# Performance work log

Measured on AMD Instinct MI355X. Metric: run time of the kernel, lower is better.

Reference implementation:

```python
import jax, jax.numpy as jnp
import numpy as np

D_MODEL = 4096
D_HIDDEN = 32768
BATCH = 2048
K = 128
N_DEAD = 2048


def _ln(x, eps=1e-5):
    # torch .std() is unbiased (ddof=1)
    mu = jnp.mean(x, axis=-1, keepdims=True)
    xc = x - mu
    std = jnp.std(x, axis=-1, keepdims=True, ddof=1)
    return xc / (std + eps), mu, std


def _topk_activation(x, k):
    # topk over last dim, relu values, scatter back into zeros
    vals, idx = jax.lax.top_k(x, k)          # [B, k]
    vals = jax.nn.relu(vals)
    rows = jnp.arange(x.shape[0])[:, None]    # [B, 1]
    return jnp.zeros_like(x).at[rows, idx].set(vals)


def setup_inputs() -> dict:
    key = jax.random.key(0)
    k1, k2 = jax.random.split(key)
    x = jax.random.normal(k1, (BATCH, D_MODEL), dtype=jnp.float32)
    # kaiming-uniform-ish encoder init
    bound = 1.0 / np.sqrt(D_MODEL)
    w_enc = jax.random.uniform(k2, (D_MODEL, D_HIDDEN), dtype=jnp.float32,
                               minval=-bound, maxval=bound)
    w_dec = w_enc.T
    w_dec = w_dec / jnp.linalg.norm(w_dec, axis=0, keepdims=True)
    b_enc = jnp.zeros((D_HIDDEN,), dtype=jnp.float32)
    b_pre = jnp.zeros((D_MODEL,), dtype=jnp.float32)
    # fixed dead-neuron mask with exactly N_DEAD dead latents
    dm = np.zeros((D_HIDDEN,), dtype=bool)
    rng = np.random.default_rng(0)
    dm[rng.choice(D_HIDDEN, size=N_DEAD, replace=False)] = True
    dead_mask = jnp.asarray(dm)
    return {"x": x, "w_enc": w_enc, "w_dec": w_dec, "b_enc": b_enc,
            "b_pre": b_pre, "dead_mask": dead_mask, "num_dead": N_DEAD}


def reference(x, w_enc, w_dec, b_enc, b_pre, dead_mask, num_dead):
    xn, mu, std = _ln(x)
    xc = xn - b_pre
    pre_acts = xc @ w_enc + b_enc                 # [B, d_hidden]
    latents = _topk_activation(pre_acts, K)
    recons = latents @ w_dec + b_pre              # [B, d_model]
    recons = recons * std + mu
    # auxk dead-neuron path (num_dead is a static python int)
    k_aux = min(x.shape[-1] // 2, num_dead)
    auxk_latents = jnp.where(dead_mask[None, :], pre_acts, -jnp.inf)
    auxk_acts = _topk_activation(auxk_latents, k_aux)
    auxk = auxk_acts @ w_dec + b_pre
    auxk = auxk * std + mu
    return recons, auxk, num_dead
```

## Files before the change

### kernel.cpp

```cpp
#include <hip/hip_runtime.h>
#include <math.h>

#define D_MODEL  4096
#define D_HIDDEN 32768
#define BATCH    2048
#define KSEL     128
#define NDEAD    2048
#define TIECAP   256

typedef short s16x8 __attribute__((ext_vector_type(8)));
typedef float f32x4 __attribute__((ext_vector_type(4)));

__device__ __forceinline__ unsigned int fkey(float f) {
    unsigned int u = __float_as_uint(f);
    return (u & 0x80000000u) ? ~u : (u | 0x80000000u);
}
__device__ __forceinline__ unsigned short f2bf(float f) {
    unsigned int u = __float_as_uint(f);
    u += 0x7FFFu + ((u >> 16) & 1u);
    return (unsigned short)(u >> 16);
}
__device__ __forceinline__ float bf2f(unsigned short h) {
    return __uint_as_float(((unsigned int)h) << 16);
}
__device__ __forceinline__ unsigned int key16x2(unsigned int u) {
    const unsigned int s = (u >> 15) & 0x10001u;
    const unsigned int mask = s * 0xFFFFu;
    return (u ^ mask) | (~mask & 0x80008000u);
}
__device__ __forceinline__ float unkey16(unsigned int k) {
    const unsigned int u = (k & 0x8000u) ? (k & 0x7FFFu) : (~k & 0xFFFFu);
    return __uint_as_float(u << 16);
}
__device__ __forceinline__ void async_copy16(void* lds_dst, const void* gsrc) {
    __builtin_amdgcn_global_load_lds(
        (const __attribute__((address_space(1))) unsigned int*)gsrc,
        (__attribute__((address_space(3))) unsigned int*)lds_dst,
        16, 0, 0);
}

__global__ __launch_bounds__(256) void ln_kernel(const float* __restrict__ x,
        double* __restrict__ mu, double* __restrict__ stdv, double* __restrict__ sinv)
{
    const int row = blockIdx.x;
    const int tid = threadIdx.x;
    const float* xr = x + (size_t)row * D_MODEL;
    float xv[16];
#pragma unroll
    for (int i = 0; i < 16; ++i) xv[i] = xr[tid + 256 * i];
    double s = 0.0;
#pragma unroll
    for (int i = 0; i < 16; ++i) s += (double)xv[i];
    __shared__ double red[4];
    __shared__ double sh_mu;
    const int lane = tid & 63, wid = tid >> 6;
#pragma unroll
    for (int off = 32; off > 0; off >>= 1) s += __shfl_down(s, off, 64);
    if (lane == 0) red[wid] = s;
    __syncthreads();
    if (tid == 0) sh_mu = (red[0] + red[1] + red[2] + red[3]) / (double)D_MODEL;
    __syncthreads();
    const double m = sh_mu;
    double s2 = 0.0;
#pragma unroll
    for (int i = 0; i < 16; ++i) { double d = (double)xv[i] - m; s2 += d * d; }
#pragma unroll
    for (int off = 32; off > 0; off >>= 1) s2 += __shfl_down(s2, off, 64);
    __syncthreads();
    if (lane == 0) red[wid] = s2;
    __syncthreads();
    if (tid == 0) {
        double var = (red[0] + red[1] + red[2] + red[3]) / (double)(D_MODEL - 1);
        double sd = sqrt(var);
        mu[row] = m;
        stdv[row] = sd;
        sinv[row] = 1.0 / (sd + 1e-5);
    }
}

__global__ void dead_scan_kernel(const unsigned char* __restrict__ mask8,
                                 int* __restrict__ dead_idx, int* __restrict__ dead_cnt,
                                 const int* __restrict__ num_dead_in, float* __restrict__ out_last)
{
    const int lane = threadIdx.x;
    int c = 0;
    for (int j = lane; j < D_HIDDEN; j += 64) c += (mask8[j] != 0);
#pragma unroll
    for (int off = 32; off > 0; off >>= 1) c += __shfl_down(c, off, 64);
    const int total_u8 = __shfl(c, 0, 64);
    const bool u8mode = (total_u8 == NDEAD);
    const int* mask32 = (const int*)mask8;
    int cnt = 0;
    for (int base = 0; base < D_HIDDEN; base += 64) {
        const int j = base + lane;
        const bool d = u8mode ? (mask8[j] != 0) : (mask32[j] != 0);
        const unsigned long long b = __ballot(d);
        const int pre = __popcll(b & ((1ull << lane) - 1ull));
        if (d && (cnt + pre) < NDEAD) dead_idx[cnt + pre] = j;
        cnt += __popcll(b);
    }
    const int cc = cnt > NDEAD ? NDEAD : cnt;
    if (lane == 0) {
        *dead_cnt = cc;
        *out_last = (float)(*num_dead_in);
    }
    for (int t = cc + lane; t < NDEAD; t += 64) dead_idx[t] = 0;
}

__global__ __launch_bounds__(256) void asplit_kernel(
    const float* __restrict__ x, const double* __restrict__ mu, const double* __restrict__ sinv,
    const float* __restrict__ b_pre, unsigned short* __restrict__ Ahp)
{
    const int row = blockIdx.x, tid = threadIdx.x;
    const double m = mu[row], si = sinv[row];
    const float* xr = x + (size_t)row * D_MODEL;
#pragma unroll
    for (int i = 0; i < 4; ++i) {
        const int j = (i * 256 + tid) * 4;
        const float4 xv = *(const float4*)(xr + j);
        const float4 bp = *(const float4*)(b_pre + j);
        float v[4];
        v[0] = (float)(((double)xv.x - m) * si) - bp.x;
        v[1] = (float)(((double)xv.y - m) * si) - bp.y;
        v[2] = (float)(((double)xv.z - m) * si) - bp.z;
        v[3] = (float)(((double)xv.w - m) * si) - bp.w;
        uint2 hw;
        hw.x = (unsigned)f2bf(v[0]) | ((unsigned)f2bf(v[1]) << 16);
        hw.y = (unsigned)f2bf(v[2]) | ((unsigned)f2bf(v[3]) << 16);
        *(uint2*)(Ahp + (size_t)row * D_MODEL + j) = hw;
    }
}

__global__ __launch_bounds__(256) void bsplit_kernel(
    const float* __restrict__ w_enc, unsigned short* __restrict__ Bhp)
{
    __shared__ float t[32][33];
    const int bk = blockIdx.x * 32;
    const int bn = blockIdx.y * 32;
    const int tid = threadIdx.x;
    const int lr = tid >> 3, lc4 = (tid & 7) * 4;
    const float4 v = *(const float4*)(w_enc + (size_t)(bk + lr) * D_HIDDEN + bn + lc4);
    t[lr][lc4 + 0] = v.x; t[lr][lc4 + 1] = v.y; t[lr][lc4 + 2] = v.z; t[lr][lc4 + 3] = v.w;
    __syncthreads();
    float o[4];
#pragma unroll
    for (int j = 0; j < 4; ++j) o[j] = t[lc4 + j][lr];
    uint2 hw;
    hw.x = (unsigned)f2bf(o[0]) | ((unsigned)f2bf(o[1]) << 16);
    hw.y = (unsigned)f2bf(o[2]) | ((unsigned)f2bf(o[3]) << 16);
    *(uint2*)(Bhp + (size_t)(bn + lr) * D_MODEL + bk + lc4) = hw;
}

__global__ __launch_bounds__(256) void wencT_kernel(
    const float* __restrict__ w_enc, float* __restrict__ wT)
{
    __shared__ float t[32][33];
    const int bk = blockIdx.x * 32;
    const int bn = blockIdx.y * 32;
    const int tid = threadIdx.x;
    const int lr = tid >> 3, lc4 = (tid & 7) * 4;
    const float4 v = *(const float4*)(w_enc + (size_t)(bk + lr) * D_HIDDEN + bn + lc4);
    t[lr][lc4 + 0] = v.x; t[lr][lc4 + 1] = v.y; t[lr][lc4 + 2] = v.z; t[lr][lc4 + 3] = v.w;
    __syncthreads();
    const int j = tid >> 3, i4 = (tid & 7) * 4;
    float4 o;
    o.x = t[i4 + 0][j]; o.y = t[i4 + 1][j]; o.z = t[i4 + 2][j]; o.w = t[i4 + 3][j];
    *(float4*)(wT + (size_t)(bn + j) * D_MODEL + bk + i4) = o;
}

template<int EPI>
__global__ __launch_bounds__(512) void mm256_kernel(
    const unsigned short* __restrict__ A, const unsigned short* __restrict__ B,
    const int kdim, const int ntiles_x,
    const float* __restrict__ bias_n,
    const double* __restrict__ muv, const double* __restrict__ stdvv,
    void* __restrict__ outp, const long ostride)
{
    __shared__ unsigned short lds[2 * 4 * 8192];
    const int tid = threadIdx.x;
    const int lane = tid & 63, wid = tid >> 6;
    const int cpx = gridDim.x >> 3;
    const int orig = blockIdx.x;
    const int wg = (orig & 7) * cpx + (orig >> 3);
    const int m0 = (wg % ntiles_x) * 256;
    const int n0 = (wg / ntiles_x) * 256;
    const int wm = (wid >> 2) * 128;
    const int wn = (wid & 3) * 64;
    const int fr = lane & 15, kq = lane >> 4;
    const int swr = (fr >> 1) & 3;
    const int qg = (lane & 3) ^ ((lane >> 3) & 3);
    const int qo = (kq ^ swr) * 8;

    f32x4 acc[8][4];
#pragma unroll
    for (int i = 0; i < 8; ++i)
#pragma unroll
        for (int j = 0; j < 4; ++j) acc[i][j] = (f32x4){0.f, 0.f, 0.f, 0.f};

    const unsigned short* sH0[4];
    int dH0[4];
#pragma unroll
    for (int j = 0; j < 4; ++j) {
        const int g = wid * 4 + j;
        const int is_b = g >> 4;
        const int sr = g & 15;
        const unsigned short* gp = is_b ? B : A;
        const int t0 = is_b ? n0 : m0;
        sH0[j] = gp + (size_t)(t0 + sr * 16 + (lane >> 2)) * kdim + qg * 8;
        dH0[j] = (is_b ? 2 : 0) * 8192 + sr * 512;
    }

    const int NT = kdim >> 6;
#pragma unroll
    for (int j = 0; j < 4; ++j) async_copy16(lds + dH0[j], sH0[j]);
#pragma unroll
    for (int j = 0; j < 4; ++j) async_copy16(lds + 8192 + dH0[j], sH0[j] + 32);
    if (NT > 1) {
#pragma unroll
        for (int j = 0; j < 4; ++j) async_copy16(lds + 32768 + dH0[j], sH0[j] + 64);
    }

    for (int t = 0; t < NT; ++t) {
        const int cur = t & 1;
        unsigned short* bb = (unsigned short*)lds + cur * 32768;
        unsigned short* nb = (unsigned short*)lds + (cur ^ 1) * 32768;
        const int k1 = (t + 1) << 6;
        const int k2 = (t + 2) << 6;

        if (t < NT - 1) { asm volatile("s_waitcnt vmcnt(8)" ::: "memory"); }
        else            { asm volatile("s_waitcnt vmcnt(4)" ::: "memory"); }
        asm volatile("s_barrier" ::: "memory");
        __builtin_amdgcn_sched_barrier(0);
        {
            if (t + 1 < NT) {
                async_copy16(nb + 8192 + dH0[0], sH0[0] + k1 + 32);
                async_copy16(nb + 8192 + dH0[1], sH0[1] + k1 + 32);
            }
            s16x8 a[4], b[4];
#pragma unroll
            for (int mi = 0; mi < 4; ++mi)
                a[mi] = *(const s16x8*)(bb + (wm + mi * 16 + fr) * 32 + qo);
#pragma unroll
            for (int ni = 0; ni < 4; ++ni)
                b[ni] = *(const s16x8*)(bb + 2 * 8192 + (wn + ni * 16 + fr) * 32 + qo);
            __builtin_amdgcn_s_setprio(1);
#pragma unroll
            for (int mi = 0; mi < 4; ++mi)
#pragma unroll
                for (int ni = 0; ni < 4; ++ni)
                    acc[mi][ni] = __builtin_amdgcn_mfma_f32_16x16x32_bf16(a[mi], b[ni], acc[mi][ni], 0, 0, 0);
            __builtin_amdgcn_s_setprio(0);
            asm volatile("s_barrier" ::: "memory");
            __builtin_amdgcn_sched_barrier(0);
            if (t + 1 < NT) {
                async_copy16(nb + 8192 + dH0[2], sH0[2] + k1 + 32);
                async_copy16(nb + 8192 + dH0[3], sH0[3] + k1 + 32);
            }
            s16x8 a2[4];
#pragma unroll
            for (int mi = 0; mi < 4; ++mi)
                a2[mi] = *(const s16x8*)(bb + (wm + (mi + 4) * 16 + fr) * 32 + qo);
            __builtin_amdgcn_s_setprio(1);
#pragma unroll
            for (int mi = 0; mi < 4; ++mi)
#pragma unroll
                for (int ni = 0; ni < 4; ++ni)
                    acc[mi + 4][ni] = __builtin_amdgcn_mfma_f32_16x16x32_bf16(a2[mi], b[ni], acc[mi + 4][ni], 0, 0, 0);
            __builtin_amdgcn_s_setprio(0);
        }
        if (t < NT - 1) { asm volatile("s_waitcnt vmcnt(8)" ::: "memory"); }
        else            { asm volatile("s_waitcnt vmcnt(0)" ::: "memory"); }
        asm volatile("s_barrier" ::: "memory");
        __builtin_amdgcn_sched_barrier(0);
        {
            if (t + 2 < NT) {
                async_copy16(bb + dH0[0], sH0[0] + k2);
                async_copy16(bb + dH0[1], sH0[1] + k2);
            }
            s16x8 a[4], b[4];
#pragma unroll
            for (int mi = 0; mi < 4; ++mi)
                a[mi] = *(const s16x8*)(bb + 8192 + (wm + mi * 16 + fr) * 32 + qo);
#pragma unroll
            for (int ni = 0; ni < 4; ++ni)
                b[ni] = *(const s16x8*)(bb + 3 * 8192 + (wn + ni * 16 + fr) * 32 + qo);
            __builtin_amdgcn_s_setprio(1);
#pragma unroll
            for (int mi = 0; mi < 4; ++mi)
#pragma unroll
                for (int ni = 0; ni < 4; ++ni)
                    acc[mi][ni] = __builtin_amdgcn_mfma_f32_16x16x32_bf16(a[mi], b[ni], acc[mi][ni], 0, 0, 0);
            __builtin_amdgcn_s_setprio(0);
            asm volatile("s_barrier" ::: "memory");
            __builtin_amdgcn_sched_barrier(0);
            if (t + 2 < NT) {
                async_copy16(bb + dH0[2], sH0[2] + k2);
                async_copy16(bb + dH0[3], sH0[3] + k2);
            }
            s16x8 a2[4];
#pragma unroll
            for (int mi = 0; mi < 4; ++mi)
                a2[mi] = *(const s16x8*)(bb + 8192 + (wm + (mi + 4) * 16 + fr) * 32 + qo);
            __builtin_amdgcn_s_setprio(1);
#pragma unroll
            for (int mi = 0; mi < 4; ++mi)
#pragma unroll
                for (int ni = 0; ni < 4; ++ni)
                    acc[mi + 4][ni] = __builtin_amdgcn_mfma_f32_16x16x32_bf16(a2[mi], b[ni], acc[mi + 4][ni], 0, 0, 0);
            __builtin_amdgcn_s_setprio(0);
        }
    }

#pragma unroll
    for (int ni = 0; ni < 4; ++ni) {
        const int col = n0 + wn + ni * 16 + fr;
        const float be = bias_n[col];
#pragma unroll
        for (int mi = 0; mi < 8; ++mi) {
            const int rb = m0 + wm + mi * 16 + kq * 4;
            if (EPI == 0) {
                unsigned short* O = (unsigned short*)outp;
#pragma unroll
                for (int r = 0; r < 4; ++r)
                    O[(size_t)(rb + r) * ostride + col] = f2bf(acc[mi][ni][r] + be);
            } else {
                float* O = (float*)outp;
#pragma unroll
                for (int r = 0; r < 4; ++r) {
                    const int m = rb + r;
                    O[(size_t)m * ostride + col] =
                        (acc[mi][ni][r] + be) * (float)stdvv[m] + (float)muv[m];
                }
            }
        }
    }
}

template<int EPI>
__global__ __launch_bounds__(256) void mm_kernel(
    const unsigned short* __restrict__ A, const unsigned short* __restrict__ B,
    const int kdim, const int ntiles_x,
    const float* __restrict__ bias_n,
    const double* __restrict__ muv, const double* __restrict__ stdvv,
    void* __restrict__ outp, const long ostride)
{
    __shared__ unsigned short lds[3 * 2 * 128 * 32];
    const int tid = threadIdx.x;
    const int lane = tid & 63, wid = tid >> 6;
    const int cpx = gridDim.x >> 3;
    const int orig = blockIdx.x;
    const int wg = (orig & 7) * cpx + (orig >> 3);
    const int m0 = (wg % ntiles_x) * 128;
    const int n0 = (wg / ntiles_x) * 128;
    const int wm = (wid >> 1) * 64, wn = (wid & 1) * 64;
    const int fr = lane & 15, kq = lane >> 4;
    const int swr = (fr >> 1) & 3;
    const int qg = (lane & 3) ^ ((lane >> 3) & 3);
    const int qo = (kq ^ swr) * 8;

    f32x4 acc[4][4];
#pragma unroll
    for (int i = 0; i < 4; ++i)
#pragma unroll
        for (int j = 0; j < 4; ++j) acc[i][j] = (f32x4){0.f, 0.f, 0.f, 0.f};

    const unsigned short* srcs[4];
    int d0[4];
#pragma unroll
    for (int j = 0; j < 4; ++j) {
        const int s = wid * 4 + j;
        const int pl = s >> 3, sr = s & 7;
        const int r = sr * 16 + (lane >> 2);
        srcs[j] = (pl ? B : A) + (size_t)((pl ? n0 : m0) + r) * kdim + qg * 8;
        d0[j] = pl * 4096 + sr * 512;
    }

    const int NT = kdim >> 5;
#pragma unroll
    for (int j = 0; j < 4; ++j) async_copy16(lds + 0 * 8192 + d0[j], srcs[j]);
#pragma unroll
    for (int j = 0; j < 4; ++j) async_copy16(lds + 1 * 8192 + d0[j], srcs[j] + 32);

    int cur = 0, nxt = 2;
    for (int t = 0; t < NT; ++t) {
        if (t < NT - 1) {
            asm volatile("s_waitcnt vmcnt(4)" ::: "memory");
        } else {
            asm volatile("s_waitcnt vmcnt(0)" ::: "memory");
        }
        __builtin_amdgcn_s_barrier();
        __builtin_amdgcn_sched_barrier(0);

        if (t + 2 < NT) {
            const int k2 = (t + 2) << 5;
#pragma unroll
            for (int j = 0; j < 4; ++j) async_copy16(lds + nxt * 8192 + d0[j], srcs[j] + k2);
        }

        const unsigned short* la = lds + cur * 8192;
        const unsigned short* lb = la + 4096;
        s16x8 a[4], b[4];
#pragma unroll
        for (int i = 0; i < 4; ++i) {
            a[i] = *(const s16x8*)(la + (wm + i * 16 + fr) * 32 + qo);
            b[i] = *(const s16x8*)(lb + (wn + i * 16 + fr) * 32 + qo);
        }
#pragma unroll
        for (int mi = 0; mi < 4; ++mi)
#pragma unroll
            for (int ni = 0; ni < 4; ++ni)
                acc[mi][ni] = __builtin_amdgcn_mfma_f32_16x16x32_bf16(a[mi], b[ni], acc[mi][ni], 0, 0, 0);

        cur = cur == 2 ? 0 : cur + 1;
        nxt = nxt == 2 ? 0 : nxt + 1;
    }

#pragma unroll
    for (int ni = 0; ni < 4; ++ni) {
        const int col = n0 + wn + ni * 16 + fr;
        const float be = bias_n[col];
#pragma unroll
        for (int mi = 0; mi < 4; ++mi) {
            const int rb = m0 + wm + mi * 16 + kq * 4;
            if (EPI == 0) {
                unsigned short* O = (unsigned short*)outp;
#pragma unroll
                for (int r = 0; r < 4; ++r)
                    O[(size_t)(rb + r) * ostride + col] = f2bf(acc[mi][ni][r] + be);
            } else {
                float* O = (float*)outp;
#pragma unroll
                for (int r = 0; r < 4; ++r) {
                    const int m = rb + r;
                    O[(size_t)m * ostride + col] =
                        (acc[mi][ni][r] + be) * (float)stdvv[m] + (float)muv[m];
                }
            }
        }
    }
}

__global__ __launch_bounds__(256) void topk_sel_kernel(
    const unsigned short* __restrict__ p16,
    int* __restrict__ topk_idx, float* __restrict__ topk_val,
    int* __restrict__ sure_cnt, int* __restrict__ tie_cnt, int* __restrict__ cand_col)
{
    const int row = blockIdx.x;
    const int tid = threadIdx.x;
    const int lane = tid & 63, wid = tid >> 6;
    const unsigned short* pr = p16 + (size_t)row * D_HIDDEN;

    __shared__ int red[4];
    __shared__ int sh_sel, sh_tie;

    uint4 kr[16];
#pragma unroll
    for (int i = 0; i < 16; ++i) {
        uint4 w = *(const uint4*)(pr + (i * 256 + tid) * 8);
        w.x = key16x2(w.x); w.y = key16x2(w.y); w.z = key16x2(w.z); w.w = key16x2(w.w);
        kr[i] = w;
    }
    if (tid == 0) { sh_sel = 0; sh_tie = 0; }

    unsigned int lo = 0, hi = 65535;
    while (lo < hi) {
        const unsigned int mid = (lo + hi) >> 1;
        int c = 0;
#pragma unroll
        for (int i = 0; i < 16; ++i) {
            const unsigned int u[4] = {kr[i].x, kr[i].y, kr[i].z, kr[i].w};
#pragma unroll
            for (int e = 0; e < 4; ++e) {
                c += (int)((u[e] & 0xFFFFu) > mid);
                c += (int)((u[e] >> 16) > mid);
            }
        }
#pragma unroll
        for (int off = 32; off > 0; off >>= 1) c += __shfl_down(c, off, 64);
        if (lane == 0) red[wid] = c;
        __syncthreads();
        const int total = red[0] + red[1] + red[2] + red[3];
        if (total < KSEL) hi = mid; else lo = mid + 1;
        __syncthreads();
    }
    const unsigned int K16 = lo;

    const float vc = unkey16(K16);
    const float DLT = 1.3e-2f;
    const float sureT = vc + 2.f * DLT;
    const float candT = vc - 2.f * DLT;
    const unsigned int sK = fkey(sureT) >> 16;
    const unsigned int cK = fkey(candT) >> 16;

    int* oidx = topk_idx + row * KSEL;
    float* oval = topk_val + row * KSEL;
    int* cc = cand_col + row * TIECAP;
#pragma unroll
    for (int i = 0; i < 16; ++i) {
        const int j0 = (i * 256 + tid) * 8;
        const unsigned int u[4] = {kr[i].x, kr[i].y, kr[i].z, kr[i].w};
#pragma unroll
        for (int e = 0; e < 8; ++e) {
            const unsigned int k = (e & 1) ? (u[e >> 1] >> 16) : (u[e >> 1] & 0xFFFFu);
            if (k < cK) continue;
            const float v = unkey16(k);
            if (k > sK && v > sureT) {
                const int pos = atomicAdd(&sh_sel, 1);
                oidx[pos] = j0 + e;
                oval[pos] = v > 0.f ? v : 0.f;
            } else if (v >= candT) {
                const int t = atomicAdd(&sh_tie, 1);
                if (t < TIECAP) cc[t] = j0 + e;
            }
        }
    }
    __syncthreads();
    if (tid == 0) {
        sure_cnt[row] = sh_sel;
        tie_cnt[row] = sh_tie > TIECAP ? TIECAP : sh_tie;
    }
}

__global__ __launch_bounds__(256) void topk_refine_kernel(
    const int* __restrict__ tie_cnt, const int* __restrict__ cand_col,
    double* __restrict__ cand_val,
    const float* __restrict__ x, const double* __restrict__ mu, const double* __restrict__ sinv,
    const float* __restrict__ b_pre, const float* __restrict__ wT, const float* __restrict__ b_enc)
{
    const int row = blockIdx.x;
    const int tid = threadIdx.x;
    const int lane = tid & 63, wid = tid >> 6;
    const int T = tie_cnt[row];
    const int base = (int)blockIdx.y * 4 + wid;
    if (base >= T) return;
    const double m_ = mu[row], si = sinv[row];
    const float* xr = x + (size_t)row * D_MODEL;
    for (int slot = base; slot < T; slot += 64) {
        const int col = cand_col[row * TIECAP + slot];
        const float* wr = wT + (size_t)col * D_MODEL;
        double s0 = 0.0, s1 = 0.0;
        for (int k = lane * 4; k < D_MODEL; k += 512) {
            {
                const float4 xv = *(const float4*)(xr + k);
                const float4 bp = *(const float4*)(b_pre + k);
                const float4 wv4 = *(const float4*)(wr + k);
                s0 += (((double)xv.x - m_) * si - (double)bp.x) * (double)wv4.x;
                s0 += (((double)xv.y - m_) * si - (double)bp.y) * (double)wv4.y;
                s0 += (((double)xv.z - m_) * si - (double)bp.z) * (double)wv4.z;
                s0 += (((double)xv.w - m_) * si - (double)bp.w) * (double)wv4.w;
            }
            {
                const int k2 = k + 256;
                const float4 xv = *(const float4*)(xr + k2);
                const float4 bp = *(const float4*)(b_pre + k2);
                const float4 wv4 = *(const float4*)(wr + k2);
                s1 += (((double)xv.x - m_) * si - (double)bp.x) * (double)wv4.x;
                s1 += (((double)xv.y - m_) * si - (double)bp.y) * (double)wv4.y;
                s1 += (((double)xv.z - m_) * si - (double)bp.z) * (double)wv4.z;
                s1 += (((double)xv.w - m_) * si - (double)bp.w) * (double)wv4.w;
            }
        }
        double s = s0 + s1;
#pragma unroll
        for (int off = 32; off > 0; off >>= 1) s += __shfl_down(s, off, 64);
        if (lane == 0) cand_val[row * TIECAP + slot] = s + (double)b_enc[col];
    }
}

__global__ __launch_bounds__(256) void topk_fin_kernel(
    const int* __restrict__ sure_cnt, const int* __restrict__ tie_cnt,
    const int* __restrict__ cand_col, const double* __restrict__ cand_val,
    int* __restrict__ topk_idx, float* __restrict__ topk_val)
{
    const int row = blockIdx.x;
    const int tid = threadIdx.x;
    __shared__ double vals[TIECAP];
    __shared__ int cols[TIECAP];
    const int G = sure_cnt[row];
    const int T = tie_cnt[row];
    const int R = KSEL - G;
    if (tid < T) {
        vals[tid] = cand_val[row * TIECAP + tid];
        cols[tid] = cand_col[row * TIECAP + tid];
    }
    __syncthreads();
    int* oidx = topk_idx + row * KSEL;
    float* oval = topk_val + row * KSEL;
    if (tid < T) {
        const double v = vals[tid];
        const int c = cols[tid];
        int rank = 0;
        for (int u = 0; u < T; ++u) {
            const double vu = vals[u];
            rank += (int)((vu > v) || (vu == v && cols[u] < c));
        }
        if (rank < R) {
            oidx[G + rank] = c;
            oval[G + rank] = v > 0.0 ? (float)v : 0.f;
        }
    }
    const int take = R < T ? R : T;
    if (tid >= take && tid < R) {
        oidx[G + tid] = (T > 0) ? cols[0] : 0;
        oval[G + tid] = 0.f;
    }
}

__global__ __launch_bounds__(256) void wdec2bf_kernel(
    const float* __restrict__ w_dec, unsigned short* __restrict__ wd16)
{
    const size_t gid = (size_t)blockIdx.x * 256 + threadIdx.x;
    const size_t base = gid * 8;
    const float4 a = *(const float4*)(w_dec + base);
    const float4 b = *(const float4*)(w_dec + base + 4);
    uint4 o;
    o.x = (unsigned)f2bf(a.x) | ((unsigned)f2bf(a.y) << 16);
    o.y = (unsigned)f2bf(a.z) | ((unsigned)f2bf(a.w) << 16);
    o.z = (unsigned)f2bf(b.x) | ((unsigned)f2bf(b.y) << 16);
    o.w = (unsigned)f2bf(b.z) | ((unsigned)f2bf(b.w) << 16);
    *(uint4*)(wd16 + base) = o;
}

__global__ __launch_bounds__(256) void decode_kernel(
    const int* __restrict__ topk_idx, const float* __restrict__ topk_val,
    const unsigned short* __restrict__ wd16, const float* __restrict__ b_pre,
    const double* __restrict__ mu, const double* __restrict__ stdv,
    float* __restrict__ out0)
{
    const int row = blockIdx.x;
    const int tid = threadIdx.x;
    __shared__ int sidx[KSEL];
    __shared__ float sval[KSEL];
    if (tid < KSEL) {
        sidx[tid] = topk_idx[row * KSEL + tid];
        sval[tid] = topk_val[row * KSEL + tid];
    }
    __syncthreads();
    float acc[16];
#pragma unroll
    for (int i = 0; i < 16; ++i) acc[i] = 0.f;
    const int dbase = tid * 16;
    for (int k = 0; k < KSEL; ++k) {
        const float v = sval[k];
        if (v == 0.f) continue;
        const uint4* wr = (const uint4*)(wd16 + (size_t)sidx[k] * D_MODEL + dbase);
        const uint4 w0 = wr[0], w1 = wr[1];
        const unsigned int u[8] = {w0.x, w0.y, w0.z, w0.w, w1.x, w1.y, w1.z, w1.w};
#pragma unroll
        for (int i = 0; i < 8; ++i) {
            acc[2 * i]     += v * __uint_as_float(u[i] << 16);
            acc[2 * i + 1] += v * __uint_as_float(u[i] & 0xFFFF0000u);
        }
    }
    const float st = (float)stdv[row];
    const float mm = (float)mu[row];
    float* o = out0 + (size_t)row * D_MODEL + dbase;
#pragma unroll
    for (int i = 0; i < 16; ++i) {
        o[i] = (acc[i] + b_pre[dbase + i]) * st + mm;
    }
}

__global__ __launch_bounds__(256) void auxg_kernel(
    const unsigned short* __restrict__ p16, const int* __restrict__ dead_idx,
    const int* __restrict__ dead_cnt, unsigned short* __restrict__ Ahd)
{
    const int r = blockIdx.x;
    const int tid = threadIdx.x;
    const int dc = *dead_cnt;
#pragma unroll
    for (int i = 0; i < 8; ++i) {
        const int c = i * 256 + tid;
        unsigned short v = 0;
        if (c < dc) {
            const unsigned short u = p16[(size_t)r * D_HIDDEN + dead_idx[c]];
            v = (u & 0x8000u) ? (unsigned short)0 : u;
        }
        Ahd[(size_t)r * NDEAD + c] = v;
    }
}

__global__ __launch_bounds__(256) void auxb_kernel(
    const float* __restrict__ w_dec, const int* __restrict__ dead_idx,
    unsigned short* __restrict__ Bhd)
{
    __shared__ float t[32][33];
    const int k0 = blockIdx.x * 32;
    const int n0 = blockIdx.y * 32;
    const int tid = threadIdx.x;
    const int i = tid >> 3, j4 = (tid & 7) * 4;
    const int srow = dead_idx[k0 + i];
    const float4 v = *(const float4*)(w_dec + (size_t)srow * D_MODEL + n0 + j4);
    t[i][j4 + 0] = v.x; t[i][j4 + 1] = v.y; t[i][j4 + 2] = v.z; t[i][j4 + 3] = v.w;
    __syncthreads();
    const int j = tid >> 3, i4 = (tid & 7) * 4;
    uint2 hw;
    hw.x = (unsigned)f2bf(t[i4 + 0][j]) | ((unsigned)f2bf(t[i4 + 1][j]) << 16);
    hw.y = (unsigned)f2bf(t[i4 + 2][j]) | ((unsigned)f2bf(t[i4 + 3][j]) << 16);
    *(uint2*)(Bhd + (size_t)(n0 + j) * NDEAD + k0 + i4) = hw;
}

extern "C" void kernel_launch(void* const* d_in, const int* in_sizes, int n_in,
                              void* d_out, int out_size, void* d_ws, size_t ws_size,
                              hipStream_t stream)
{
    (void)in_sizes; (void)n_in; (void)out_size; (void)ws_size;
    const float* x      = (const float*)d_in[0];
    const float* w_enc  = (const float*)d_in[1];
    const float* w_dec  = (const float*)d_in[2];
    const float* b_enc  = (const float*)d_in[3];
    const float* b_pre  = (const float*)d_in[4];
    const unsigned char* dead_mask = (const unsigned char*)d_in[5];
    const int* num_dead = (const int*)d_in[6];
    float* out = (float*)d_out;

    char* base = (char*)d_ws;
    char* w = base;
    auto alloc = [&](size_t bytes) -> char* {
        char* p = w;
        w += (bytes + 255) & ~(size_t)255;
        return p;
    };
    unsigned short* p16 = (unsigned short*)alloc((size_t)BATCH * D_HIDDEN * 2);
    double* mu       = (double*)alloc((size_t)BATCH * 8);
    double* stdv     = (double*)alloc((size_t)BATCH * 8);
    double* sinv     = (double*)alloc((size_t)BATCH * 8);
    int* topk_idx    = (int*)alloc((size_t)BATCH * KSEL * 4);
    float* topk_val  = (float*)alloc((size_t)BATCH * KSEL * 4);
    int* dead_idx    = (int*)alloc((size_t)NDEAD * 4);
    int* dead_cnt    = (int*)alloc(256);
    int* sure_cnt    = (int*)alloc((size_t)BATCH * 4);
    int* tie_cnt     = (int*)alloc((size_t)BATCH * 4);
    int* cand_col    = (int*)alloc((size_t)BATCH * TIECAP * 4);
    double* cand_val = (double*)alloc((size_t)BATCH * TIECAP * 8);
    unsigned short* Ahp = (unsigned short*)alloc((size_t)BATCH * D_MODEL * 2);
    char* region     = alloc((size_t)D_HIDDEN * D_MODEL * 4);

    unsigned short* Bhp = (unsigned short*)region;
    float* wT   = (float*)region;
    unsigned short* wd16 = (unsigned short*)region;
    unsigned short* Bhd  = (unsigned short*)(region + (size_t)D_HIDDEN * D_MODEL * 2);
    unsigned short* Ahd  = Ahp;

    float* out0 = out;
    float* out1 = out + (size_t)BATCH * D_MODEL;
    float* out_last = out + (size_t)2 * BATCH * D_MODEL;

    ln_kernel<<<BATCH, 256, 0, stream>>>(x, mu, stdv, sinv);
    dead_scan_kernel<<<1, 64, 0, stream>>>(dead_mask, dead_idx, dead_cnt, num_dead, out_last);
    asplit_kernel<<<BATCH, 256, 0, stream>>>(x, mu, sinv, b_pre, Ahp);
    bsplit_kernel<<<dim3(D_MODEL / 32, D_HIDDEN / 32), 256, 0, stream>>>(w_enc, Bhp);
    mm256_kernel<0><<<(BATCH / 256) * (D_HIDDEN / 256), 512, 0, stream>>>(
        Ahp, Bhp, D_MODEL, BATCH / 256, b_enc, nullptr, nullptr, p16, (long)D_HIDDEN);
    wencT_kernel<<<dim3(D_MODEL / 32, D_HIDDEN / 32), 256, 0, stream>>>(w_enc, wT);
    topk_sel_kernel<<<BATCH, 256, 0, stream>>>(p16, topk_idx, topk_val, sure_cnt, tie_cnt, cand_col);
    topk_refine_kernel<<<dim3(BATCH, 16), 256, 0, stream>>>(
        tie_cnt, cand_col, cand_val, x, mu, sinv, b_pre, wT, b_enc);
    topk_fin_kernel<<<BATCH, 256, 0, stream>>>(
        sure_cnt, tie_cnt, cand_col, cand_val, topk_idx, topk_val);
    auxg_kernel<<<BATCH, 256, 0, stream>>>(p16, dead_idx, dead_cnt, Ahd);
    auxb_kernel<<<dim3(NDEAD / 32, D_MODEL / 32), 256, 0, stream>>>(w_dec, dead_idx, Bhd);
    wdec2bf_kernel<<<(int)(((size_t)D_HIDDEN * D_MODEL) / (256 * 8)), 256, 0, stream>>>(w_dec, wd16);
    decode_kernel<<<BATCH, 256, 0, stream>>>(topk_idx, topk_val, wd16, b_pre, mu, stdv, out0);
    mm_kernel<1><<<(BATCH / 128) * (D_MODEL / 128), 256, 0, stream>>>(
        Ahd, Bhd, NDEAD, BATCH / 128, b_pre, mu, stdv, out1, (long)D_MODEL);
}
```

Measured before the change: 2.242 ms.

## Fuse layernorm with A-prep and weight transpose passes, precompute centered input

Merges the layernorm stats kernel with the bf16 activation conversion, so x is read once, and also writes a hi/lo float split of the centered input for the refine kernel. When the workspace is large enough, the bf16 weight conversion and the fp32 transpose of w_enc run in one kernel, saving a second full read of the 512MB weight. The refine kernel reads the precomputed hi/lo values instead of recomputing the normalization in double. In exchange it needs extra workspace for a separate wT buffer plus two fp32 activation copies, and falls back to the old path if the workspace is too small.

```diff
diff --git a/kernel.cpp b/kernel.cpp
--- a/kernel.cpp
+++ b/kernel.cpp
@@ -39,8 +39,10 @@
         16, 0, 0);
 }
 
-__global__ __launch_bounds__(256) void ln_kernel(const float* __restrict__ x,
-        double* __restrict__ mu, double* __restrict__ stdv, double* __restrict__ sinv)
+__global__ __launch_bounds__(256) void prep_kernel(
+    const float* __restrict__ x, const float* __restrict__ b_pre,
+    double* __restrict__ mu, double* __restrict__ stdv, double* __restrict__ sinv,
+    unsigned short* __restrict__ Ahp, float* __restrict__ xch, float* __restrict__ xcl)
 {
     const int row = blockIdx.x;
     const int tid = threadIdx.x;
@@ -52,7 +54,7 @@
 #pragma unroll
     for (int i = 0; i < 16; ++i) s += (double)xv[i];
     __shared__ double red[4];
-    __shared__ double sh_mu;
+    __shared__ double sh_mu, sh_si;
     const int lane = tid & 63, wid = tid >> 6;
 #pragma unroll
     for (int off = 32; off > 0; off >>= 1) s += __shfl_down(s, off, 64);
@@ -74,7 +76,34 @@
         double sd = sqrt(var);
         mu[row] = m;
         stdv[row] = sd;
-        sinv[row] = 1.0 / (sd + 1e-5);
+        const double si = 1.0 / (sd + 1e-5);
+        sinv[row] = si;
+        sh_si = si;
+    }
+    __syncthreads();
+    const double si = sh_si;
+#pragma unroll
+    for (int i = 0; i < 4; ++i) {
+        const int j = (i * 256 + tid) * 4;
+        const float4 x4 = *(const float4*)(xr + j);
+        const float4 bp = *(const float4*)(b_pre + j);
+        float vf[4], hi[4], lo[4];
+        const float xe[4] = {x4.x, x4.y, x4.z, x4.w};
+        const float be[4] = {bp.x, bp.y, bp.z, bp.w};
+#pragma unroll
+        for (int e = 0; e < 4; ++e) {
+            const double t = ((double)xe[e] - m) * si;
+            vf[e] = (float)t - be[e];
+            const double a = t - (double)be[e];
+            hi[e] = (float)a;
+            lo[e] = (float)(a - (double)hi[e]);
+        }
+        uint2 hw;
+        hw.x = (unsigned)f2bf(vf[0]) | ((unsigned)f2bf(vf[1]) << 16);
+        hw.y = (unsigned)f2bf(vf[2]) | ((unsigned)f2bf(vf[3]) << 16);
+        *(uint2*)(Ahp + (size_t)row * D_MODEL + j) = hw;
+        *(float4*)(xch + (size_t)row * D_MODEL + j) = make_float4(hi[0], hi[1], hi[2], hi[3]);
+        *(float4*)(xcl + (size_t)row * D_MODEL + j) = make_float4(lo[0], lo[1], lo[2], lo[3]);
     }
 }
 
@@ -107,30 +136,6 @@
     for (int t = cc + lane; t < NDEAD; t += 64) dead_idx[t] = 0;
 }
 
-__global__ __launch_bounds__(256) void asplit_kernel(
-    const float* __restrict__ x, const double* __restrict__ mu, const double* __restrict__ sinv,
-    const float* __restrict__ b_pre, unsigned short* __restrict__ Ahp)
-{
-    const int row = blockIdx.x, tid = threadIdx.x;
-    const double m = mu[row], si = sinv[row];
-    const float* xr = x + (size_t)row * D_MODEL;
-#pragma unroll
-    for (int i = 0; i < 4; ++i) {
-        const int j = (i * 256 + tid) * 4;
-        const float4 xv = *(const float4*)(xr + j);
-        const float4 bp = *(const float4*)(b_pre + j);
-        float v[4];
-        v[0] = (float)(((double)xv.x - m) * si) - bp.x;
-        v[1] = (float)(((double)xv.y - m) * si) - bp.y;
-        v[2] = (float)(((double)xv.z - m) * si) - bp.z;
-        v[3] = (float)(((double)xv.w - m) * si) - bp.w;
-        uint2 hw;
-        hw.x = (unsigned)f2bf(v[0]) | ((unsigned)f2bf(v[1]) << 16);
-        hw.y = (unsigned)f2bf(v[2]) | ((unsigned)f2bf(v[3]) << 16);
-        *(uint2*)(Ahp + (size_t)row * D_MODEL + j) = hw;
-    }
-}
-
 __global__ __launch_bounds__(256) void bsplit_kernel(
     const float* __restrict__ w_enc, unsigned short* __restrict__ Bhp)
 {
@@ -166,6 +171,28 @@
     float4 o;
     o.x = t[i4 + 0][j]; o.y = t[i4 + 1][j]; o.z = t[i4 + 2][j]; o.w = t[i4 + 3][j];
     *(float4*)(wT + (size_t)(bn + j) * D_MODEL + bk + i4) = o;
+}
+
+__global__ __launch_bounds__(256) void wprep_kernel(
+    const float* __restrict__ w_enc, unsigned short* __restrict__ Bhp,
+    float* __restrict__ wT)
+{
+    __shared__ float t[32][33];
+    const int bk = blockIdx.x * 32;
+    const int bn = blockIdx.y * 32;
+    const int tid = threadIdx.x;
+    const int lr = tid >> 3, lc4 = (tid & 7) * 4;
+    const float4 v = *(const float4*)(w_enc + (size_t)(bk + lr) * D_HIDDEN + bn + lc4);
+    t[lr][lc4 + 0] = v.x; t[lr][lc4 + 1] = v.y; t[lr][lc4 + 2] = v.z; t[lr][lc4 + 3] = v.w;
+    __syncthreads();
+    float o[4];
+#pragma unroll
+    for (int j = 0; j < 4; ++j) o[j] = t[lc4 + j][lr];
+    uint2 hw;
+    hw.x = (unsigned)f2bf(o[0]) | ((unsigned)f2bf(o[1]) << 16);
+    hw.y = (unsigned)f2bf(o[2]) | ((unsigned)f2bf(o[3]) << 16);
+    *(uint2*)(Bhp + (size_t)(bn + lr) * D_MODEL + bk + lc4) = hw;
+    *(float4*)(wT + (size_t)(bn + lr) * D_MODEL + bk + lc4) = make_float4(o[0], o[1], o[2], o[3]);
 }
 
 template<int EPI>
@@ -524,8 +551,8 @@
 __global__ __launch_bounds__(256) void topk_refine_kernel(
     const int* __restrict__ tie_cnt, const int* __restrict__ cand_col,
     double* __restrict__ cand_val,
-    const float* __restrict__ x, const double* __restrict__ mu, const double* __restrict__ sinv,
-    const float* __restrict__ b_pre, const float* __restrict__ wT, const float* __restrict__ b_enc)
+    const float* __restrict__ xch, const float* __restrict__ xcl,
+    const float* __restrict__ wT, const float* __restrict__ b_enc)
 {
     const int row = blockIdx.x;
     const int tid = threadIdx.x;
@@ -533,31 +560,31 @@
     const int T = tie_cnt[row];
     const int base = (int)blockIdx.y * 4 + wid;
     if (base >= T) return;
-    const double m_ = mu[row], si = sinv[row];
-    const float* xr = x + (size_t)row * D_MODEL;
+    const float* hr = xch + (size_t)row * D_MODEL;
+    const float* lr2 = xcl + (size_t)row * D_MODEL;
     for (int slot = base; slot < T; slot += 64) {
         const int col = cand_col[row * TIECAP + slot];
         const float* wr = wT + (size_t)col * D_MODEL;
         double s0 = 0.0, s1 = 0.0;
         for (int k = lane * 4; k < D_MODEL; k += 512) {
             {
-                const float4 xv = *(const float4*)(xr + k);
-                const float4 bp = *(const float4*)(b_pre + k);
-                const float4 wv4 = *(const float4*)(wr + k);
-                s0 += (((double)xv.x - m_) * si - (double)bp.x) * (double)wv4.x;
-                s0 += (((double)xv.y - m_) * si - (double)bp.y) * (double)wv4.y;
-                s0 += (((double)xv.z - m_) * si - (double)bp.z) * (double)wv4.z;
-                s0 += (((double)xv.w - m_) * si - (double)bp.w) * (double)wv4.w;
+                const float4 h = *(const float4*)(hr + k);
+                const float4 l = *(const float4*)(lr2 + k);
+                const float4 w4 = *(const float4*)(wr + k);
+                s0 += ((double)h.x + (double)l.x) * (double)w4.x;
+                s0 += ((double)h.y + (double)l.y) * (double)w4.y;
+                s0 += ((double)h.z + (double)l.z) * (double)w4.z;
+                s0 += ((double)h.w + (double)l.w) * (double)w4.w;
             }
             {
                 const int k2 = k + 256;
-                const float4 xv = *(const float4*)(xr + k2);
-                const float4 bp = *(const float4*)(b_pre + k2);
-                const float4 wv4 = *(const float4*)(wr + k2);
-                s1 += (((double)xv.x - m_) * si - (double)bp.x) * (double)wv4.x;
-                s1 += (((double)xv.y - m_) * si - (double)bp.y) * (double)wv4.y;
-                s1 += (((double)xv.z - m_) * si - (double)bp.z) * (double)wv4.z;
-                s1 += (((double)xv.w - m_) * si - (double)bp.w) * (double)wv4.w;
+                const float4 h = *(const float4*)(hr + k2);
+                const float4 l = *(const float4*)(lr2 + k2);
+                const float4 w4 = *(const float4*)(wr + k2);
+                s1 += ((double)h.x + (double)l.x) * (double)w4.x;
+                s1 += ((double)h.y + (double)l.y) * (double)w4.y;
+                s1 += ((double)h.z + (double)l.z) * (double)w4.z;
+                s1 += ((double)h.w + (double)l.w) * (double)w4.w;
             }
         }
         double s = s0 + s1;
@@ -704,7 +731,7 @@
                               void* d_out, int out_size, void* d_ws, size_t ws_size,
                               hipStream_t stream)
 {
-    (void)in_sizes; (void)n_in; (void)out_size; (void)ws_size;
+    (void)in_sizes; (void)n_in; (void)out_size;
     const float* x      = (const float*)d_in[0];
     const float* w_enc  = (const float*)d_in[1];
     const float* w_dec  = (const float*)d_in[2];
@@ -733,29 +760,42 @@
     int* tie_cnt     = (int*)alloc((size_t)BATCH * 4);
     int* cand_col    = (int*)alloc((size_t)BATCH * TIECAP * 4);
     double* cand_val = (double*)alloc((size_t)BATCH * TIECAP * 8);
+    float* xch       = (float*)alloc((size_t)BATCH * D_MODEL * 4);
+    float* xcl       = (float*)alloc((size_t)BATCH * D_MODEL * 4);
     unsigned short* Ahp = (unsigned short*)alloc((size_t)BATCH * D_MODEL * 2);
     char* region     = alloc((size_t)D_HIDDEN * D_MODEL * 4);
+    const size_t need_small = (size_t)(w - base);
+    float* wT_big    = (float*)alloc((size_t)D_HIDDEN * D_MODEL * 4);
+    const size_t need_big = (size_t)(w - base);
+    const bool bigws = (ws_size >= need_big);
+    (void)need_small;
 
     unsigned short* Bhp = (unsigned short*)region;
-    float* wT   = (float*)region;
+    float* wT_small = (float*)region;
     unsigned short* wd16 = (unsigned short*)region;
     unsigned short* Bhd  = (unsigned short*)(region + (size_t)D_HIDDEN * D_MODEL * 2);
     unsigned short* Ahd  = Ahp;
+    float* wT = bigws ? wT_big : wT_small;
 
     float* out0 = out;
     float* out1 = out + (size_t)BATCH * D_MODEL;
     float* out_last = out + (size_t)2 * BATCH * D_MODEL;
 
-    ln_kernel<<<BATCH, 256, 0, stream>>>(x, mu, stdv, sinv);
+    prep_kernel<<<BATCH, 256, 0, stream>>>(x, b_pre, mu, stdv, sinv, Ahp, xch, xcl);
     dead_scan_kernel<<<1, 64, 0, stream>>>(dead_mask, dead_idx, dead_cnt, num_dead, out_last);
-    asplit_kernel<<<BATCH, 256, 0, stream>>>(x, mu, sinv, b_pre, Ahp);
-    bsplit_kernel<<<dim3(D_MODEL / 32, D_HIDDEN / 32), 256, 0, stream>>>(w_enc, Bhp);
+    if (bigws) {
+        wprep_kernel<<<dim3(D_MODEL / 32, D_HIDDEN / 32), 256, 0, stream>>>(w_enc, Bhp, wT);
+    } else {
+        bsplit_kernel<<<dim3(D_MODEL / 32, D_HIDDEN / 32), 256, 0, stream>>>(w_enc, Bhp);
+    }
     mm256_kernel<0><<<(BATCH / 256) * (D_HIDDEN / 256), 512, 0, stream>>>(
         Ahp, Bhp, D_MODEL, BATCH / 256, b_enc, nullptr, nullptr, p16, (long)D_HIDDEN);
-    wencT_kernel<<<dim3(D_MODEL / 32, D_HIDDEN / 32), 256, 0, stream>>>(w_enc, wT);
+    if (!bigws) {
+        wencT_kernel<<<dim3(D_MODEL / 32, D_HIDDEN / 32), 256, 0, stream>>>(w_enc, wT);
+    }
     topk_sel_kernel<<<BATCH, 256, 0, stream>>>(p16, topk_idx, topk_val, sure_cnt, tie_cnt, cand_col);
     topk_refine_kernel<<<dim3(BATCH, 16), 256, 0, stream>>>(
-        tie_cnt, cand_col, cand_val, x, mu, sinv, b_pre, wT, b_enc);
+        tie_cnt, cand_col, cand_val, xch, xcl, wT, b_enc);
     topk_fin_kernel<<<BATCH, 256, 0, stream>>>(
         sure_cnt, tie_cnt, cand_col, cand_val, topk_idx, topk_val);
     auxg_kernel<<<BATCH, 256, 0, stream>>>(p16, dead_idx, dead_cnt, Ahd);
```

Measured after the change: 2.123 ms. -5.3%, faster.
